# Performance work log

Hardware: AMD Instinct MI355X
Metric: run time of the kernel (lower is better)

The kernel has to match this reference:

```python
import jax, jax.numpy as jnp
import numpy as np

E = 1024  # embed_dim

def setup_inputs() -> dict:
    key = jax.random.key(0)
    ks = jax.random.split(key, 7)
    s = 1.0 / np.sqrt(E)  # torch Linear default init scale (uniform bound)
    x = jax.random.normal(ks[0], (4, 2048, E), dtype=jnp.float32)
    Wq = jax.random.uniform(ks[1], (E, E), jnp.float32, -s, s)
    bq = jax.random.uniform(ks[2], (E,), jnp.float32, -s, s)
    Wk = jax.random.uniform(ks[3], (E, E), jnp.float32, -s, s)
    bk = jax.random.uniform(ks[4], (E,), jnp.float32, -s, s)
    Wv = jax.random.uniform(ks[5], (E, E), jnp.float32, -s, s)
    bv = jax.random.uniform(ks[6], (E,), jnp.float32, -s, s)
    return {"x": x, "Wq": Wq, "bq": bq, "Wk": Wk, "bk": bk, "Wv": Wv, "bv": bv}

def reference(x, Wq, bq, Wk, bk, Wv, bv):
    # torch nn.Linear: y = x @ W.T + b
    Q = jnp.einsum('bse,fe->bsf', x, Wq) + bq
    K = jnp.einsum('bse,fe->bsf', x, Wk) + bk
    V = jnp.einsum('bse,fe->bsf', x, Wv) + bv
    scale = jnp.sqrt(jnp.asarray(E, x.dtype))
    scores = jnp.einsum('bqd,bkd->bqk', Q, K) / scale  # [B,S,S]
    attn = jax.nn.softmax(scores, axis=-1)
    return jnp.einsum('bqk,bkd->bqd', attn, V)
```

## Files before the change

kernel.cpp:

```cpp
#include <hip/hip_runtime.h>
#include <hip/hip_bf16.h>


typedef __attribute__((ext_vector_type(8))) short bf16x8;
typedef __attribute__((ext_vector_type(4))) float f32x4;

#define DEVI static __device__ __forceinline__

DEVI short to_bf16(float f) {
    unsigned u = __builtin_bit_cast(unsigned, f);
    u += 0x7fffu + ((u >> 16) & 1u);
    return (short)(u >> 16);
}
DEVI float from_bf16(short s) {
    return __builtin_bit_cast(float, (unsigned)((unsigned short)s) << 16);
}

DEVI void gload_lds16(const short* g, short* l) {
    __builtin_amdgcn_global_load_lds(
        (const __attribute__((address_space(1))) void*)g,
        (__attribute__((address_space(3))) void*)l, 16, 0, 0);
}

template<int BIAS, int EPI, typename TOUT>
__global__ __launch_bounds__(256, 3)
void gemm97(const short* __restrict__ A, long lda, long bsA,
            const short* __restrict__ B, long ldb, long bsB,
            const float* __restrict__ b0, const float* __restrict__ b1,
            const float* __restrict__ b2,
            TOUT* __restrict__ c0, TOUT* __restrict__ c1, TOUT* __restrict__ c2,
            long ldc, long bsC, int K, float scale,
            const float* __restrict__ rs, long rsLD)
{
    __shared__ __align__(16) short As[128 * 64];
    __shared__ __align__(16) short Bs[128 * 64];

    const int tid = threadIdx.x;
    const int z = blockIdx.z;

    const int gx = gridDim.x;
    const int nwg = gx * gridDim.y;
    const int id = blockIdx.y * gx + blockIdx.x;
    const int id2 = (id & 7) * (nwg >> 3) + (id >> 3);
    const long m0 = (long)(id2 / gx) * 128;
    const long n0 = (long)(id2 % gx) * 128;

    const short* Ab = A + (long)z * bsA + m0 * lda;
    const short* Bb = B + (long)z * bsB + n0 * ldb;

    const int wv = tid >> 6;
    const int lane = tid & 63;
    const int wr = (wv >> 1) * 64;
    const int wc = (wv & 1) * 64;
    const int lrow = lane & 15;
    const int q = lane >> 4;

    const int NT = K >> 6;

    auto stage = [&](int t) {
        const long k0 = (long)t * 64;
        #pragma unroll
        for (int i = 0; i < 4; ++i) {
            int s = i * 256 + tid;
            int row = s >> 3;
            int src = (s & 7) ^ (row & 7);
            gload_lds16(Ab + (long)row * lda + k0 + src * 8, &As[s * 8]);
        }
        #pragma unroll
        for (int i = 0; i < 4; ++i) {
            int s = i * 256 + tid;
            int row = s >> 3;
            int src = (s & 7) ^ (row & 7);
            gload_lds16(Bb + (long)row * ldb + k0 + src * 8, &Bs[s * 8]);
        }
    };

    f32x4 acc[4][4] = {};

    for (int t = 0; t < NT; ++t) {
        if (t) {
            asm volatile("s_waitcnt lgkmcnt(0)" ::: "memory");
            __builtin_amdgcn_sched_barrier(0);
            __builtin_amdgcn_s_barrier();
        }
        stage(t);
        asm volatile("s_waitcnt vmcnt(0)" ::: "memory");
        __builtin_amdgcn_sched_barrier(0);
        __builtin_amdgcn_s_barrier();

        bf16x8 af[4][2], bf[4][2];
        #pragma unroll
        for (int m = 0; m < 4; ++m) {
            int row = wr + m * 16 + lrow;
            #pragma unroll
            for (int kk = 0; kk < 2; ++kk) {
                int ch = (kk * 4 + q) ^ (row & 7);
                af[m][kk] = *(const bf16x8*)&As[row * 64 + ch * 8];
            }
        }
        #pragma unroll
        for (int n = 0; n < 4; ++n) {
            int row = wc + n * 16 + lrow;
            #pragma unroll
            for (int kk = 0; kk < 2; ++kk) {
                int ch = (kk * 4 + q) ^ (row & 7);
                bf[n][kk] = *(const bf16x8*)&Bs[row * 64 + ch * 8];
            }
        }

        __builtin_amdgcn_s_setprio(1);
        #pragma unroll
        for (int m = 0; m < 4; ++m)
            #pragma unroll
            for (int n = 0; n < 4; ++n)
                #pragma unroll
                for (int kk = 0; kk < 2; ++kk)
                    acc[m][n] = __builtin_amdgcn_mfma_f32_16x16x32_bf16(
                        af[m][kk], bf[n][kk], acc[m][n], 0, 0, 0);
        __builtin_amdgcn_s_setprio(0);
    }

    const float* bias = (BIAS == 2) ? b0
                      : ((z == 0) ? b0 : (z == 1) ? b1 : b2);
    TOUT* Cz = ((z == 0) ? c0 : (z == 1) ? c1 : c2) + (long)z * bsC;
    TOUT* Cb = Cz + m0 * ldc + n0;
    #pragma unroll
    for (int m = 0; m < 4; ++m) {
        #pragma unroll
        for (int r = 0; r < 4; ++r) {
            int row = wr + m * 16 + q * 4 + r;
            float iv = 1.0f;
            if constexpr (EPI == 2)
                iv = 1.0f / rs[(long)z * rsLD + m0 + row];
            #pragma unroll
            for (int n = 0; n < 4; ++n) {
                int col = wc + n * 16 + lrow;
                float v = acc[m][n][r] * scale;
                if constexpr (BIAS == 1) v += bias[n0 + col];
                if constexpr (BIAS == 2) v += bias[m0 + row];
                if constexpr (EPI == 1) v = __expf(v);
                if constexpr (EPI == 2) v *= iv;
                if constexpr (sizeof(TOUT) == 2)
                    Cb[(long)row * ldc + col] = to_bf16(v);
                else
                    Cb[(long)row * ldc + col] = v;
            }
        }
    }
}

__global__ __launch_bounds__(256)
void cvt_f32_bf16(const float* __restrict__ src, short* __restrict__ dst, int n8)
{
    int i = blockIdx.x * 256 + threadIdx.x;
    if (i < n8) {
        float4 a = ((const float4*)src)[2 * i];
        float4 b = ((const float4*)src)[2 * i + 1];
        bf16x8 o = { to_bf16(a.x), to_bf16(a.y), to_bf16(a.z), to_bf16(a.w),
                     to_bf16(b.x), to_bf16(b.y), to_bf16(b.z), to_bf16(b.w) };
        *(bf16x8*)&dst[i * 8] = o;
    }
}

__global__ __launch_bounds__(256)
void cvt3_f32_bf16(const float* __restrict__ s0, const float* __restrict__ s1,
                   const float* __restrict__ s2, short* __restrict__ dst, int n8)
{
    int zz = blockIdx.y;
    const float* src = (zz == 0) ? s0 : (zz == 1) ? s1 : s2;
    int i = blockIdx.x * 256 + threadIdx.x;
    if (i < n8) {
        float4 a = ((const float4*)src)[2 * i];
        float4 b = ((const float4*)src)[2 * i + 1];
        bf16x8 o = { to_bf16(a.x), to_bf16(a.y), to_bf16(a.z), to_bf16(a.w),
                     to_bf16(b.x), to_bf16(b.y), to_bf16(b.z), to_bf16(b.w) };
        *(bf16x8*)&dst[(long)zz * n8 * 8 + i * 8] = o;
    }
}

__global__ __launch_bounds__(256)
void rowsum_rows(const short* __restrict__ S, float* __restrict__ rs, int ncols)
{
    const long row = blockIdx.x;
    const short* p = S + row * (long)ncols;
    const int t = threadIdx.x;

    union { bf16x8 v; short s[8]; } u;
    u.v = *(const bf16x8*)&p[t * 8];
    float sum = 0.f;
    #pragma unroll
    for (int j = 0; j < 8; ++j) sum += from_bf16(u.s[j]);
    #pragma unroll
    for (int off = 32; off > 0; off >>= 1) sum += __shfl_xor(sum, off);

    __shared__ float red[4];
    const int wave = t >> 6;
    if ((t & 63) == 0) red[wave] = sum;
    __syncthreads();
    if (t == 0) rs[row] = red[0] + red[1] + red[2] + red[3];
}

extern "C" void kernel_launch(void* const* d_in, const int* in_sizes, int n_in,
                              void* d_out, int out_size, void* d_ws, size_t ws_size,
                              hipStream_t stream)
{
    (void)in_sizes; (void)n_in; (void)out_size; (void)ws_size;

    const float* x  = (const float*)d_in[0];
    const float* Wq = (const float*)d_in[1];
    const float* bq = (const float*)d_in[2];
    const float* Wk = (const float*)d_in[3];
    const float* bk = (const float*)d_in[4];
    const float* Wv = (const float*)d_in[5];
    const float* bv = (const float*)d_in[6];
    float* out = (float*)d_out;

    const int S = 2048, E = 1024;
    const long M1 = 1024l * 1024;

    short* w  = (short*)d_ws;
    short* Q  = w;
    short* Kb = w + 8 * M1;
    short* P  = w + 16 * M1;
    float* rs = (float*)w;
    short* VT = w + 8 * M1;

    short* dows = (short*)d_out;
    short* xb = dows;
    short* Wb = dows + 8 * M1;

    dim3 blk(256);

    cvt_f32_bf16<<<dim3(4096), blk, 0, stream>>>(x, xb, (int)M1);
    cvt3_f32_bf16<<<dim3(512, 3), blk, 0, stream>>>(Wq, Wk, Wv, Wb, (int)(M1 / 8));

    gemm97<1, 0, short><<<dim3(8, 64, 2), blk, 0, stream>>>(
        xb, E, 0, Wb, E, M1, bq, bk, nullptr, Q, Kb, nullptr, E, 0, E, 1.0f,
        nullptr, 0);

    gemm97<0, 1, short><<<dim3(16, 16, 4), blk, 0, stream>>>(
        Q, E, 2 * M1, Kb, E, 2 * M1, nullptr, nullptr, nullptr,
        P, P, P, S, 4 * M1, E, 0.03125f, nullptr, 0);

    gemm97<2, 0, short><<<dim3(16, 8, 4), blk, 0, stream>>>(
        Wb + 2 * M1, E, 0, xb, E, 2 * M1, bv, nullptr, nullptr,
        VT, VT, VT, S, 2 * M1, E, 1.0f, nullptr, 0);

    rowsum_rows<<<dim3(4 * S), blk, 0, stream>>>(P, rs, S);

    gemm97<0, 2, float><<<dim3(8, 16, 4), blk, 0, stream>>>(
        P, S, 4 * M1, VT, S, 2 * M1, nullptr, nullptr, nullptr,
        out, out, out, E, 2 * M1, S, 1.0f, rs, S);
}
```

Before: 182.4 us.

## Fuse softmax row-sum partials into QK^T epilogue and merge conversion kernels

The exp epilogue of the QK^T GEMM now also accumulates per-row partial sums through lane shuffles and writes them to a scratch buffer. A small reduce kernel then combines the 32 partials per row, which removes the separate rowsum pass that re-read the whole bf16 P matrix. The x and weight fp32-to-bf16 conversions are merged into one launch. The trade-off is extra shuffles and stores in the GEMM epilogue, plus a partial-sum buffer placed in the output region. The sums are taken over unrounded fp32 exp values, while the GEMM that follows uses the bf16-rounded P.

```diff
diff --git a/kernel.cpp b/kernel.cpp
--- a/kernel.cpp
+++ b/kernel.cpp
@@ -30,7 +30,7 @@
             const float* __restrict__ b2,
             TOUT* __restrict__ c0, TOUT* __restrict__ c1, TOUT* __restrict__ c2,
             long ldc, long bsC, int K, float scale,
-            const float* __restrict__ rs, long rsLD)
+            const float* __restrict__ rs, long rsLD, float* __restrict__ ps)
 {
     __shared__ __align__(16) short As[128 * 64];
     __shared__ __align__(16) short Bs[128 * 64];
@@ -132,72 +132,69 @@
             float iv = 1.0f;
             if constexpr (EPI == 2)
                 iv = 1.0f / rs[(long)z * rsLD + m0 + row];
+            float rsum = 0.f;
             #pragma unroll
             for (int n = 0; n < 4; ++n) {
                 int col = wc + n * 16 + lrow;
                 float v = acc[m][n][r] * scale;
                 if constexpr (BIAS == 1) v += bias[n0 + col];
                 if constexpr (BIAS == 2) v += bias[m0 + row];
-                if constexpr (EPI == 1) v = __expf(v);
+                if constexpr (EPI == 1) { v = __expf(v); rsum += v; }
                 if constexpr (EPI == 2) v *= iv;
                 if constexpr (sizeof(TOUT) == 2)
                     Cb[(long)row * ldc + col] = to_bf16(v);
                 else
                     Cb[(long)row * ldc + col] = v;
             }
+            if constexpr (EPI == 1) {
+                rsum += __shfl_xor(rsum, 1);
+                rsum += __shfl_xor(rsum, 2);
+                rsum += __shfl_xor(rsum, 4);
+                rsum += __shfl_xor(rsum, 8);
+                if (lrow == 0) {
+                    int j = (int)(n0 >> 7) * 2 + (wc >> 6);
+                    ps[((long)z * 32 + j) * 2048 + m0 + row] = rsum;
+                }
+            }
         }
     }
 }
 
 __global__ __launch_bounds__(256)
-void cvt_f32_bf16(const float* __restrict__ src, short* __restrict__ dst, int n8)
-{
-    int i = blockIdx.x * 256 + threadIdx.x;
-    if (i < n8) {
-        float4 a = ((const float4*)src)[2 * i];
-        float4 b = ((const float4*)src)[2 * i + 1];
-        bf16x8 o = { to_bf16(a.x), to_bf16(a.y), to_bf16(a.z), to_bf16(a.w),
-                     to_bf16(b.x), to_bf16(b.y), to_bf16(b.z), to_bf16(b.w) };
-        *(bf16x8*)&dst[i * 8] = o;
+void cvt_all(const float* __restrict__ x,
+             const float* __restrict__ wq, const float* __restrict__ wk,
+             const float* __restrict__ wv, short* __restrict__ dst)
+{
+    const int y = blockIdx.y;
+    const float* src;
+    long dstOff8;
+    long i;
+    if (y < 8) {
+        src = x;
+        i = ((long)y * 512 + blockIdx.x) * 256 + threadIdx.x;
+        dstOff8 = 0;
+    } else {
+        src = (y == 8) ? wq : (y == 9) ? wk : wv;
+        i = (long)blockIdx.x * 256 + threadIdx.x;
+        dstOff8 = (8l * 1024 * 1024 + (long)(y - 8) * 1024 * 1024) / 8;
     }
+    float4 a = ((const float4*)src)[2 * i];
+    float4 b = ((const float4*)src)[2 * i + 1];
+    bf16x8 o = { to_bf16(a.x), to_bf16(a.y), to_bf16(a.z), to_bf16(a.w),
+                 to_bf16(b.x), to_bf16(b.y), to_bf16(b.z), to_bf16(b.w) };
+    *(bf16x8*)&dst[(dstOff8 + i) * 8] = o;
 }
 
 __global__ __launch_bounds__(256)
-void cvt3_f32_bf16(const float* __restrict__ s0, const float* __restrict__ s1,
-                   const float* __restrict__ s2, short* __restrict__ dst, int n8)
-{
-    int zz = blockIdx.y;
-    const float* src = (zz == 0) ? s0 : (zz == 1) ? s1 : s2;
-    int i = blockIdx.x * 256 + threadIdx.x;
-    if (i < n8) {
-        float4 a = ((const float4*)src)[2 * i];
-        float4 b = ((const float4*)src)[2 * i + 1];
-        bf16x8 o = { to_bf16(a.x), to_bf16(a.y), to_bf16(a.z), to_bf16(a.w),
-                     to_bf16(b.x), to_bf16(b.y), to_bf16(b.z), to_bf16(b.w) };
-        *(bf16x8*)&dst[(long)zz * n8 * 8 + i * 8] = o;
-    }
-}
-
-__global__ __launch_bounds__(256)
-void rowsum_rows(const short* __restrict__ S, float* __restrict__ rs, int ncols)
-{
-    const long row = blockIdx.x;
-    const short* p = S + row * (long)ncols;
-    const int t = threadIdx.x;
-
-    union { bf16x8 v; short s[8]; } u;
-    u.v = *(const bf16x8*)&p[t * 8];
-    float sum = 0.f;
+void reduce_rs(const float* __restrict__ ps, float* __restrict__ rs)
+{
+    int row = blockIdx.x * 256 + threadIdx.x;
+    int z = row >> 11, r = row & 2047;
+    const float* p = ps + (long)z * 32 * 2048 + r;
+    float s = 0.f;
     #pragma unroll
-    for (int j = 0; j < 8; ++j) sum += from_bf16(u.s[j]);
-    #pragma unroll
-    for (int off = 32; off > 0; off >>= 1) sum += __shfl_xor(sum, off);
-
-    __shared__ float red[4];
-    const int wave = t >> 6;
-    if ((t & 63) == 0) red[wave] = sum;
-    __syncthreads();
-    if (t == 0) rs[row] = red[0] + red[1] + red[2] + red[3];
+    for (int j = 0; j < 32; ++j) s += p[j * 2048];
+    rs[row] = s;
 }
 
 extern "C" void kernel_launch(void* const* d_in, const int* in_sizes, int n_in,
@@ -228,27 +225,27 @@
     short* dows = (short*)d_out;
     short* xb = dows;
     short* Wb = dows + 8 * M1;
+    float* psum = (float*)(dows + 11 * M1);
 
     dim3 blk(256);
 
-    cvt_f32_bf16<<<dim3(4096), blk, 0, stream>>>(x, xb, (int)M1);
-    cvt3_f32_bf16<<<dim3(512, 3), blk, 0, stream>>>(Wq, Wk, Wv, Wb, (int)(M1 / 8));
+    cvt_all<<<dim3(512, 11), blk, 0, stream>>>(x, Wq, Wk, Wv, xb);
 
     gemm97<1, 0, short><<<dim3(8, 64, 2), blk, 0, stream>>>(
         xb, E, 0, Wb, E, M1, bq, bk, nullptr, Q, Kb, nullptr, E, 0, E, 1.0f,
-        nullptr, 0);
+        nullptr, 0, nullptr);
 
     gemm97<0, 1, short><<<dim3(16, 16, 4), blk, 0, stream>>>(
         Q, E, 2 * M1, Kb, E, 2 * M1, nullptr, nullptr, nullptr,
-        P, P, P, S, 4 * M1, E, 0.03125f, nullptr, 0);
+        P, P, P, S, 4 * M1, E, 0.03125f, nullptr, 0, psum);
 
     gemm97<2, 0, short><<<dim3(16, 8, 4), blk, 0, stream>>>(
         Wb + 2 * M1, E, 0, xb, E, 2 * M1, bv, nullptr, nullptr,
-        VT, VT, VT, S, 2 * M1, E, 1.0f, nullptr, 0);
-
-    rowsum_rows<<<dim3(4 * S), blk, 0, stream>>>(P, rs, S);
+        VT, VT, VT, S, 2 * M1, E, 1.0f, nullptr, 0, nullptr);
+
+    reduce_rs<<<dim3(32), blk, 0, stream>>>(psum, rs);
 
     gemm97<0, 2, float><<<dim3(8, 16, 4), blk, 0, stream>>>(
         P, S, 4 * M1, VT, S, 2 * M1, nullptr, nullptr, nullptr,
-        out, out, out, E, 2 * M1, S, 1.0f, rs, S);
-}
+        out, out, out, E, 2 * M1, S, 1.0f, rs, S, nullptr);
+}
```

Result: no change. 179.3 us (-1.7%).
